# Optimization experiments

Hardware: AMD Instinct MI355X
Metric: run time of the kernel (lower is better)

Reference implementation:

```python
import jax, jax.numpy as jnp
import numpy as np

N = 8192        # n_nodes
F = 256         # n_features
RES_H = 512     # n_res_hidden
REP_H = 256     # n_rep_hidden
EMB = 128       # embed_dim
E = 262144      # n_edges
GAMMA = 0.1


def setup_inputs() -> dict:
    key = jax.random.key(0)
    ks = jax.random.split(key, 20)
    w = lambda k, shape, s=0.05: (jax.random.normal(k, shape, jnp.float32) * s)
    return {
        "x": jax.random.normal(ks[0], (N, F), jnp.float32),
        "edge_index": jax.random.randint(ks[1], (2, E), 0, N),
        # res_model: Linear(N,RES_H)+ReLU, Linear(RES_H,F)+ReLU
        "res_W1": w(ks[2], (N, RES_H)), "res_b1": jnp.zeros((RES_H,), jnp.float32),
        "res_W2": w(ks[3], (RES_H, F)), "res_b2": jnp.zeros((F,), jnp.float32),
        "fc_W1": w(ks[4], (F, REP_H)), "fc_b1": jnp.zeros((REP_H,), jnp.float32),
        "fc_W2": w(ks[5], (REP_H, REP_H)), "fc_b2": jnp.zeros((REP_H,), jnp.float32),
        # rep_gcn: GCNConv(F,REP_H,norm=False), GCNConv(REP_H,REP_H), GCNConv(REP_H,EMB)
        "g_W0": w(ks[6], (F, REP_H)), "g_b0": jnp.zeros((REP_H,), jnp.float32),
        "g_W1": w(ks[7], (REP_H, REP_H)), "g_b1": jnp.zeros((REP_H,), jnp.float32),
        "g_W2": w(ks[8], (REP_H, EMB)), "g_b2": jnp.zeros((EMB,), jnp.float32),
        # dec_fc: Linear(EMB,REP_H)+ReLU, Linear(REP_H,F)+ReLU
        "dec_W1": w(ks[9], (EMB, REP_H)), "dec_b1": jnp.zeros((REP_H,), jnp.float32),
        "dec_W2": w(ks[10], (REP_H, F)), "dec_b2": jnp.zeros((F,), jnp.float32),
    }


def _gcn(h, src, dst, W, b, normalize):
    """PyG GCNConv: transform then aggregate src->dst; sym-norm with self loops if normalize."""
    h = h @ W
    if normalize:
        ones = jnp.ones(src.shape[0], h.dtype)
        deg = jax.ops.segment_sum(ones, dst, num_segments=N) + 1.0  # +1 self loop
        dinv = jax.lax.rsqrt(deg)
        coef = dinv[src] * dinv[dst]
        agg = jax.ops.segment_sum(h[src] * coef[:, None], dst, num_segments=N)
        agg = agg + h * (dinv * dinv)[:, None]  # self-loop message
    else:
        agg = jax.ops.segment_sum(h[src], dst, num_segments=N)
    return agg + b


def _fwd(x, edge_index, res_W1, res_b1, res_W2, res_b2, fc_W1, fc_b1, fc_W2, fc_b2,
         g_W0, g_b0, g_W1, g_b1, g_W2, g_b2, dec_W1, dec_b1, dec_W2, dec_b2):
    relu = jax.nn.relu
    src, dst = edge_index[0], edge_index[1]
    # dense adjacency (to_dense_adj accumulates edge weights = 1)
    A = jnp.zeros((N, N), x.dtype).at[src, dst].add(1.0)
    # residual model over adjacency rows
    R = relu(relu(A @ res_W1 + res_b1) @ res_W2 + res_b2)  # [N, F]
    # GCN layer 0 (normalize=False)
    H = relu(_gcn(x, src, dst, g_W0, g_b0, False))
    # layer 1
    R_l = relu(R @ fc_W1 + fc_b1)
    H = relu(_gcn(H * jnp.exp(-GAMMA * R_l), src, dst, g_W1, g_b1, True))
    # layer 2
    R_l = relu(R_l @ fc_W2 + fc_b2)
    H = relu(_gcn(H * jnp.exp(-GAMMA * R_l), src, dst, g_W2, g_b2, True))  # [N, EMB]
    X_hat = relu(relu(H @ dec_W1 + dec_b1) @ dec_W2 + dec_b2)  # [N, F]
    A_hat = H @ H.T  # [N, N]
    return X_hat, A_hat, R


def reference(x, edge_index, res_W1, res_b1, res_W2, res_b2, fc_W1, fc_b1, fc_W2, fc_b2,
              g_W0, g_b0, g_W1, g_b1, g_W2, g_b2, dec_W1, dec_b1, dec_W2, dec_b2):
    return _fwd(x, edge_index, res_W1, res_b1, res_W2, res_b2, fc_W1, fc_b1, fc_W2, fc_b2,
                g_W0, g_b0, g_W1, g_b1, g_W2, g_b2, dec_W1, dec_b1, dec_W2, dec_b2)
```

## Files before the change

### kernel.cpp

```cpp
#include <hip/hip_runtime.h>
#include <cstddef>
#include <cstdint>
#include <math.h>

#define NN   8192
#define FF   256
#define RESH 512
#define REPH 256
#define EMBD 128
#define EE   262144
#define GAMMA_ 0.1f

typedef __attribute__((ext_vector_type(8))) short bf16x8;
typedef __attribute__((ext_vector_type(4))) float f32x4;
typedef __attribute__((ext_vector_type(2))) float f32x2;
typedef __attribute__((ext_vector_type(4))) short s16x4;
typedef __attribute__((ext_vector_type(2))) short s16x2;

__device__ inline void f2hilo(float x, short& h, short& l) {
  unsigned u = __float_as_uint(x);
  unsigned r = u + 0x7FFFu + ((u >> 16) & 1u);
  h = (short)(r >> 16);
  float hf = __uint_as_float(r & 0xFFFF0000u);
  float lf = x - hf;
  unsigned u2 = __float_as_uint(lf);
  unsigned r2 = u2 + 0x7FFFu + ((u2 >> 16) & 1u);
  l = (short)(r2 >> 16);
}


__global__ void count_kernel(const int* __restrict__ ei, int* __restrict__ cnt_src,
                             int* __restrict__ cnt_dst) {
  int e = blockIdx.x * blockDim.x + threadIdx.x;
  if (e < EE) {
    atomicAdd(&cnt_src[ei[e]], 1);
    atomicAdd(&cnt_dst[ei[EE + e]], 1);
  }
}

__global__ void scan_kernel(const int* __restrict__ cnt_src, const int* __restrict__ cnt_dst,
                            int* __restrict__ off_src, int* __restrict__ off_dst,
                            float* __restrict__ dinv) {
  const int* cnt = blockIdx.x ? cnt_dst : cnt_src;
  int* off = blockIdx.x ? off_dst : off_src;
  __shared__ int sm[1024];
  int carry = 0;
  for (int ch = 0; ch < NN / 1024; ++ch) {
    int idx = ch * 1024 + threadIdx.x;
    int v = cnt[idx];
    if (blockIdx.x) dinv[idx] = rsqrtf((float)v + 1.0f);
    int x = v;
    sm[threadIdx.x] = x;
    __syncthreads();
    for (int ofs = 1; ofs < 1024; ofs <<= 1) {
      int y = (threadIdx.x >= ofs) ? sm[threadIdx.x - ofs] : 0;
      __syncthreads();
      x += y;
      sm[threadIdx.x] = x;
      __syncthreads();
    }
    off[idx] = x - v + carry;
    carry += sm[1023];
    __syncthreads();
  }
  if (threadIdx.x == 0) off[NN] = carry;
}

__global__ void fill_kernel(const int* __restrict__ ei, const int* __restrict__ off_src,
                            const int* __restrict__ off_dst, int* __restrict__ cur_src,
                            int* __restrict__ cur_dst, int* __restrict__ adj_src,
                            int* __restrict__ adj_dst) {
  int e = blockIdx.x * blockDim.x + threadIdx.x;
  if (e < EE) {
    int s = ei[e], d = ei[EE + e];
    int ps = atomicAdd(&cur_src[s], 1);
    adj_src[off_src[s] + ps] = d;
    int pd = atomicAdd(&cur_dst[d], 1);
    adj_dst[off_dst[d] + pd] = s;
  }
}

__global__ __launch_bounds__(256) void s1_v2(const float* __restrict__ W1,
    const float* __restrict__ b1, const int* __restrict__ off_src,
    const int* __restrict__ adj_src, short* __restrict__ S1h, short* __restrict__ S1l) {
  __shared__ f32x4 p2[2][64];
  const int i = blockIdx.x, w = threadIdx.x >> 6, lane = threadIdx.x & 63;
  const int half = w & 1, par = w >> 1;
  const int col = half * 256 + lane * 4;
  const float* base = W1 + col;
  const int beg = off_src[i], end = off_src[i + 1];
  f32x4 acc = {};
  int k = beg + par;
  for (; k + 6 < end; k += 8) {
    int s0 = adj_src[k], s1 = adj_src[k + 2], s2 = adj_src[k + 4], s3 = adj_src[k + 6];
    f32x4 h0 = *(const f32x4*)(base + (size_t)s0 * RESH);
    f32x4 h1 = *(const f32x4*)(base + (size_t)s1 * RESH);
    f32x4 h2 = *(const f32x4*)(base + (size_t)s2 * RESH);
    f32x4 h3 = *(const f32x4*)(base + (size_t)s3 * RESH);
    acc += h0 + h1 + h2 + h3;
  }
  for (; k < end; k += 2) {
    int s = adj_src[k];
    acc += *(const f32x4*)(base + (size_t)s * RESH);
  }
  if (par == 1) p2[half][lane] = acc;
  __syncthreads();
  if (par == 0) {
    acc += p2[half][lane];
    f32x4 bb = *(const f32x4*)(b1 + col);
    s16x4 vh, vl;
#pragma unroll
    for (int j = 0; j < 4; ++j) {
      float v = fmaxf(acc[j] + bb[j], 0.f);
      short hh, ll;
      f2hilo(v, hh, ll);
      vh[j] = hh; vl[j] = ll;
    }
    size_t o = (size_t)i * RESH + col;
    *(s16x4*)(S1h + o) = vh;
    *(s16x4*)(S1l + o) = vl;
  }
}

__global__ __launch_bounds__(256) void agg0_v2(const float* __restrict__ h,
    const float* __restrict__ b, const float* __restrict__ mod,
    const int* __restrict__ off_dst, const int* __restrict__ adj_dst,
    short* __restrict__ oh, short* __restrict__ ol) {
  __shared__ f32x4 part[3][64];
  const int d = blockIdx.x, w = threadIdx.x >> 6, lane = threadIdx.x & 63;
  const float* base = h + lane * 4;
  const int beg = off_dst[d], end = off_dst[d + 1];
  f32x4 acc = {};
  int k = beg + w;
  for (; k + 12 < end; k += 16) {
    int s0 = adj_dst[k], s1 = adj_dst[k + 4], s2 = adj_dst[k + 8], s3 = adj_dst[k + 12];
    f32x4 h0 = *(const f32x4*)(base + (size_t)s0 * REPH);
    f32x4 h1 = *(const f32x4*)(base + (size_t)s1 * REPH);
    f32x4 h2 = *(const f32x4*)(base + (size_t)s2 * REPH);
    f32x4 h3 = *(const f32x4*)(base + (size_t)s3 * REPH);
    acc += h0 + h1 + h2 + h3;
  }
  for (; k < end; k += 4) {
    int s = adj_dst[k];
    acc += *(const f32x4*)(base + (size_t)s * REPH);
  }
  if (w) part[w - 1][lane] = acc;
  __syncthreads();
  if (w == 0) {
    acc += part[0][lane] + part[1][lane] + part[2][lane];
    size_t o = (size_t)d * REPH + lane * 4;
    f32x4 bb = *(const f32x4*)(b + lane * 4);
    f32x4 mm = *(const f32x4*)(mod + o);
    s16x4 vh, vl;
#pragma unroll
    for (int j = 0; j < 4; ++j) {
      float v = fmaxf(acc[j] + bb[j], 0.f) * expf(-GAMMA_ * mm[j]);
      short hh, ll;
      f2hilo(v, hh, ll);
      vh[j] = hh; vl[j] = ll;
    }
    *(s16x4*)(oh + o) = vh;
    *(s16x4*)(ol + o) = vl;
  }
}

__global__ __launch_bounds__(256) void aggn256_v2(const float* __restrict__ h,
    const float* __restrict__ b, const float* __restrict__ dinv,
    const float* __restrict__ mod, const int* __restrict__ off_dst,
    const int* __restrict__ adj_dst, short* __restrict__ oh, short* __restrict__ ol) {
  __shared__ f32x4 part[3][64];
  const int d = blockIdx.x, w = threadIdx.x >> 6, lane = threadIdx.x & 63;
  const float* base = h + lane * 4;
  const int beg = off_dst[d], end = off_dst[d + 1];
  f32x4 acc = {};
  int k = beg + w;
  for (; k + 12 < end; k += 16) {
    int s0 = adj_dst[k], s1 = adj_dst[k + 4], s2 = adj_dst[k + 8], s3 = adj_dst[k + 12];
    float d0 = dinv[s0], d1 = dinv[s1], d2 = dinv[s2], d3 = dinv[s3];
    f32x4 h0 = *(const f32x4*)(base + (size_t)s0 * REPH);
    f32x4 h1 = *(const f32x4*)(base + (size_t)s1 * REPH);
    f32x4 h2 = *(const f32x4*)(base + (size_t)s2 * REPH);
    f32x4 h3 = *(const f32x4*)(base + (size_t)s3 * REPH);
    acc += h0 * d0 + h1 * d1 + h2 * d2 + h3 * d3;
  }
  for (; k < end; k += 4) {
    int s = adj_dst[k];
    acc += *(const f32x4*)(base + (size_t)s * REPH) * dinv[s];
  }
  if (w) part[w - 1][lane] = acc;
  __syncthreads();
  if (w == 0) {
    acc += part[0][lane] + part[1][lane] + part[2][lane];
    const float dd = dinv[d];
    size_t o = (size_t)d * REPH + lane * 4;
    f32x4 bb = *(const f32x4*)(b + lane * 4);
    f32x4 self = *(const f32x4*)(h + o);
    s16x4 vh, vl;
    if (mod) {
      f32x4 mm = *(const f32x4*)(mod + o);
#pragma unroll
      for (int j = 0; j < 4; ++j) {
        float v = fmaxf(acc[j] * dd + self[j] * dd * dd + bb[j], 0.f) * expf(-GAMMA_ * mm[j]);
        short hh, ll; f2hilo(v, hh, ll); vh[j] = hh; vl[j] = ll;
      }
    } else {
#pragma unroll
      for (int j = 0; j < 4; ++j) {
        float v = fmaxf(acc[j] * dd + self[j] * dd * dd + bb[j], 0.f);
        short hh, ll; f2hilo(v, hh, ll); vh[j] = hh; vl[j] = ll;
      }
    }
    *(s16x4*)(oh + o) = vh;
    *(s16x4*)(ol + o) = vl;
  }
}

__global__ __launch_bounds__(256) void aggn128_v2(const float* __restrict__ h,
    const float* __restrict__ b, const float* __restrict__ dinv,
    const int* __restrict__ off_dst, const int* __restrict__ adj_dst,
    short* __restrict__ oh, short* __restrict__ ol) {
  __shared__ f32x2 part[3][64];
  const int d = blockIdx.x, w = threadIdx.x >> 6, lane = threadIdx.x & 63;
  const float* base = h + lane * 2;
  const int beg = off_dst[d], end = off_dst[d + 1];
  f32x2 acc = {};
  int k = beg + w;
  for (; k + 12 < end; k += 16) {
    int s0 = adj_dst[k], s1 = adj_dst[k + 4], s2 = adj_dst[k + 8], s3 = adj_dst[k + 12];
    float d0 = dinv[s0], d1 = dinv[s1], d2 = dinv[s2], d3 = dinv[s3];
    f32x2 h0 = *(const f32x2*)(base + (size_t)s0 * EMBD);
    f32x2 h1 = *(const f32x2*)(base + (size_t)s1 * EMBD);
    f32x2 h2 = *(const f32x2*)(base + (size_t)s2 * EMBD);
    f32x2 h3 = *(const f32x2*)(base + (size_t)s3 * EMBD);
    acc += h0 * d0 + h1 * d1 + h2 * d2 + h3 * d3;
  }
  for (; k < end; k += 4) {
    int s = adj_dst[k];
    acc += *(const f32x2*)(base + (size_t)s * EMBD) * dinv[s];
  }
  if (w) part[w - 1][lane] = acc;
  __syncthreads();
  if (w == 0) {
    acc += part[0][lane] + part[1][lane] + part[2][lane];
    const float dd = dinv[d];
    size_t o = (size_t)d * EMBD + lane * 2;
    f32x2 bb = *(const f32x2*)(b + lane * 2);
    f32x2 self = *(const f32x2*)(h + o);
    s16x2 vh, vl;
#pragma unroll
    for (int j = 0; j < 2; ++j) {
      float v = fmaxf(acc[j] * dd + self[j] * dd * dd + bb[j], 0.f);
      short hh, ll; f2hilo(v, hh, ll); vh[j] = hh; vl[j] = ll;
    }
    *(s16x2*)(oh + o) = vh;
    *(s16x2*)(ol + o) = vl;
  }
}

struct WDesc { const float* src; short* h; short* l; int K; int N; };
struct WTab { WDesc d[8]; };

__global__ void prep_w(WTab tab) {
  WDesc d = tab.d[blockIdx.y];
  int total = d.K * d.N;
  for (int i = blockIdx.x * 256 + threadIdx.x; i < total; i += 128 * 256) {
    int n = i / d.K, k = i - n * d.K;
    float x = d.src[(size_t)k * d.N + n];
    short hh, ll;
    f2hilo(x, hh, ll);
    d.h[i] = hh;
    d.l[i] = ll;
  }
}

__global__ void conv_split(const float* __restrict__ in, short* __restrict__ oh,
                           short* __restrict__ ol) {
  int i = (blockIdx.x * 256 + threadIdx.x) * 4;
  f32x4 v = *(const f32x4*)(in + i);
  s16x4 vh, vl;
#pragma unroll
  for (int j = 0; j < 4; ++j) {
    short hh, ll;
    f2hilo(v[j], hh, ll);
    vh[j] = hh;
    vl[j] = ll;
  }
  *(s16x4*)(oh + i) = vh;
  *(s16x4*)(ol + i) = vl;
}

template<int CB>
__global__ __launch_bounds__(256) void gemmS(const short* __restrict__ Ah,
    const short* __restrict__ Al, const short* __restrict__ Wh,
    const short* __restrict__ Wl, const float* __restrict__ bias, int doRelu,
    float* __restrict__ outF, short* __restrict__ outH, short* __restrict__ outL,
    int K, int Nc) {
  const int w = threadIdx.x >> 6, l = threadIdx.x & 63;
  const int lr = l & 15, lk = l >> 4;
  const int m0 = blockIdx.y * 64 + w * 16;
  const int n0 = blockIdx.x * (CB * 16);
  f32x4 acc[CB] = {};
  const int nks = K >> 5;
  for (int ks = 0; ks < nks; ++ks) {
    const int k0 = (ks << 5) + (lk << 3);
    size_t aoff = (size_t)(m0 + lr) * K + k0;
    bf16x8 ah = *(const bf16x8*)(Ah + aoff);
    bf16x8 al = *(const bf16x8*)(Al + aoff);
#pragma unroll
    for (int cb = 0; cb < CB; ++cb) {
      size_t boff = (size_t)(n0 + (cb << 4) + lr) * K + k0;
      bf16x8 bh = *(const bf16x8*)(Wh + boff);
      bf16x8 bl = *(const bf16x8*)(Wl + boff);
      acc[cb] = __builtin_amdgcn_mfma_f32_16x16x32_bf16(ah, bh, acc[cb], 0, 0, 0);
      acc[cb] = __builtin_amdgcn_mfma_f32_16x16x32_bf16(al, bh, acc[cb], 0, 0, 0);
      acc[cb] = __builtin_amdgcn_mfma_f32_16x16x32_bf16(ah, bl, acc[cb], 0, 0, 0);
    }
  }
#pragma unroll
  for (int cb = 0; cb < CB; ++cb) {
    int col = n0 + (cb << 4) + lr;
    float bv = bias ? bias[col] : 0.f;
#pragma unroll
    for (int r = 0; r < 4; ++r) {
      int row = m0 + (lk << 2) + r;
      float v = acc[cb][r] + bv;
      if (doRelu) v = fmaxf(v, 0.f);
      size_t off = (size_t)row * Nc + col;
      if (outF) outF[off] = v;
      if (outH) {
        short hh, ll;
        f2hilo(v, hh, ll);
        outH[off] = hh;
        outL[off] = ll;
      }
    }
  }
}

__global__ __launch_bounds__(256) void ahat_sym(const short* __restrict__ Hh,
    const short* __restrict__ Hl, float* __restrict__ C) {
  __shared__ float sm[128][129];
  int z = blockIdx.x;
  int b = (int)((sqrtf(8.f * (float)z + 1.f) - 1.f) * 0.5f);
  while ((b + 1) * (b + 2) / 2 <= z) ++b;
  while (b * (b + 1) / 2 > z) --b;
  int a = z - b * (b + 1) / 2;
  const int bi = a * 128, bj = b * 128;
  const bool mirror = (a != b);
  const int w = threadIdx.x >> 6, l = threadIdx.x & 63;
  const int lr = l & 15, lk = l >> 4;
  const int ri = w * 32;
  f32x4 acc[2][8] = {};
#pragma unroll
  for (int ks = 0; ks < 4; ++ks) {
    const int k0 = (ks << 5) + (lk << 3);
    bf16x8 ah[2], al[2];
#pragma unroll
    for (int rb = 0; rb < 2; ++rb) {
      size_t off = (size_t)(bi + ri + (rb << 4) + lr) * EMBD + k0;
      ah[rb] = *(const bf16x8*)(Hh + off);
      al[rb] = *(const bf16x8*)(Hl + off);
    }
#pragma unroll
    for (int cb = 0; cb < 8; ++cb) {
      size_t off = (size_t)(bj + (cb << 4) + lr) * EMBD + k0;
      bf16x8 bh = *(const bf16x8*)(Hh + off);
      bf16x8 bl = *(const bf16x8*)(Hl + off);
#pragma unroll
      for (int rb = 0; rb < 2; ++rb) {
        acc[rb][cb] = __builtin_amdgcn_mfma_f32_16x16x32_bf16(ah[rb], bh, acc[rb][cb], 0, 0, 0);
        acc[rb][cb] = __builtin_amdgcn_mfma_f32_16x16x32_bf16(al[rb], bh, acc[rb][cb], 0, 0, 0);
        acc[rb][cb] = __builtin_amdgcn_mfma_f32_16x16x32_bf16(ah[rb], bl, acc[rb][cb], 0, 0, 0);
      }
    }
  }
#pragma unroll
  for (int rb = 0; rb < 2; ++rb)
#pragma unroll
    for (int cb = 0; cb < 8; ++cb) {
      int r0 = ri + (rb << 4) + (lk << 2);
      int c0 = (cb << 4) + lr;
#pragma unroll
      for (int r = 0; r < 4; ++r) {
        float v = acc[rb][cb][r];
        C[(size_t)(bi + r0 + r) * NN + bj + c0] = v;
        if (mirror) sm[r0 + r][c0] = v;
      }
    }
  if (mirror) {
    __syncthreads();
    for (int idx = threadIdx.x; idx < 128 * 128; idx += 256) {
      int jr = idx >> 7, c = idx & 127;
      C[(size_t)(bj + jr) * NN + bi + c] = sm[c][jr];
    }
  }
}


extern "C" void kernel_launch(void* const* d_in, const int* in_sizes, int n_in,
                              void* d_out, int out_size, void* d_ws, size_t ws_size,
                              hipStream_t stream) {
  const float* x      = (const float*)d_in[0];
  const int*   ei     = (const int*)d_in[1];
  const float* res_W1 = (const float*)d_in[2];
  const float* res_b1 = (const float*)d_in[3];
  const float* res_W2 = (const float*)d_in[4];
  const float* res_b2 = (const float*)d_in[5];
  const float* fc_W1  = (const float*)d_in[6];
  const float* fc_b1  = (const float*)d_in[7];
  const float* fc_W2  = (const float*)d_in[8];
  const float* fc_b2  = (const float*)d_in[9];
  const float* g_W0   = (const float*)d_in[10];
  const float* g_b0   = (const float*)d_in[11];
  const float* g_W1   = (const float*)d_in[12];
  const float* g_b1   = (const float*)d_in[13];
  const float* g_W2   = (const float*)d_in[14];
  const float* g_b2   = (const float*)d_in[15];
  const float* dec_W1 = (const float*)d_in[16];
  const float* dec_b1 = (const float*)d_in[17];
  const float* dec_W2 = (const float*)d_in[18];
  const float* dec_b2 = (const float*)d_in[19];

  float* out   = (float*)d_out;
  float* X_hat = out;
  float* A_hat = out + (size_t)NN * FF;
  float* R     = A_hat + (size_t)NN * NN;

  char* ws = (char*)d_ws;
  size_t o = 0;
  auto alloc = [&](size_t bytes) -> void* {
    void* p = ws + o;
    o += (bytes + 1023) & ~(size_t)1023;
    return p;
  };
  int* cnt_src = (int*)alloc(NN * 4);
  int* cnt_dst = (int*)alloc(NN * 4);
  int* cur_src = (int*)alloc(NN * 4);
  int* cur_dst = (int*)alloc(NN * 4);
  int* off_src = (int*)alloc((NN + 1) * 4);
  int* off_dst = (int*)alloc((NN + 1) * 4);
  int* adj_src = (int*)alloc((size_t)EE * 4);
  int* adj_dst = (int*)alloc((size_t)EE * 4);
  float* dinv  = (float*)alloc(NN * 4);
  short* Wt_h  = (short*)alloc(524288 * 2);
  short* Wt_l  = (short*)alloc(524288 * 2);
  const size_t SLAB = (size_t)8 * 1024 * 1024;
  char* slabA = (char*)alloc(SLAB);
  char* slabB = (char*)alloc(SLAB);
  char* slabC = (char*)alloc(SLAB);
  char* slabD = (char*)alloc(SLAB);
  short* S1h = (short*)slabA;
  short* Xh  = (short*)slabA;            short* Xl  = (short*)(slabA + SLAB / 2);
  short* M1h = (short*)slabA;            short* M1l = (short*)(slabA + SLAB / 2);
  short* M2h = (short*)slabA;            short* M2l = (short*)(slabA + SLAB / 2);
  short* D1h = (short*)slabA;            short* D1l = (short*)(slabA + SLAB / 2);
  short* S1l = (short*)slabB;
  float* B3f = (float*)slabB;
  float* B4f = (float*)slabB;
  float* G2f = (float*)slabB;
  short* Rh  = (short*)slabC;            short* Rl  = (short*)(slabC + SLAB / 2);
  float* B1f = (float*)slabC;
  float* G1f = (float*)slabC;
  short* B3h = (short*)slabD;            short* B3l = (short*)(slabD + SLAB / 2);
  short* Hh  = (short*)slabD;            short* Hl  = (short*)(slabD + (size_t)2 * 1024 * 1024);

  const int o_resW2 = 0;
  const int o_fcW1  = 131072;
  const int o_fcW2  = 196608;
  const int o_gW0   = 262144;
  const int o_gW1   = 327680;
  const int o_gW2   = 393216;
  const int o_decW1 = 425984;
  const int o_decW2 = 458752;

  hipMemsetAsync(cnt_src, 0, (size_t)NN * 4 * 4, stream);

  count_kernel<<<EE / 256, 256, 0, stream>>>(ei, cnt_src, cnt_dst);
  scan_kernel<<<2, 1024, 0, stream>>>(cnt_src, cnt_dst, off_src, off_dst, dinv);
  fill_kernel<<<EE / 256, 256, 0, stream>>>(ei, off_src, off_dst, cur_src, cur_dst,
                                            adj_src, adj_dst);

  WTab tab;
  tab.d[0] = {res_W2, Wt_h + o_resW2, Wt_l + o_resW2, RESH, FF};
  tab.d[1] = {fc_W1,  Wt_h + o_fcW1,  Wt_l + o_fcW1,  FF,   REPH};
  tab.d[2] = {fc_W2,  Wt_h + o_fcW2,  Wt_l + o_fcW2,  REPH, REPH};
  tab.d[3] = {g_W0,   Wt_h + o_gW0,   Wt_l + o_gW0,   FF,   REPH};
  tab.d[4] = {g_W1,   Wt_h + o_gW1,   Wt_l + o_gW1,   REPH, REPH};
  tab.d[5] = {g_W2,   Wt_h + o_gW2,   Wt_l + o_gW2,   REPH, EMBD};
  tab.d[6] = {dec_W1, Wt_h + o_decW1, Wt_l + o_decW1, EMBD, REPH};
  tab.d[7] = {dec_W2, Wt_h + o_decW2, Wt_l + o_decW2, REPH, FF};
  prep_w<<<dim3(128, 8), 256, 0, stream>>>(tab);

  s1_v2<<<NN, 256, 0, stream>>>(res_W1, res_b1, off_src, adj_src, S1h, S1l);
  gemmS<8><<<dim3(2, 128), 256, 0, stream>>>(S1h, S1l, Wt_h + o_resW2, Wt_l + o_resW2,
      res_b2, 1, R, Rh, Rl, RESH, FF);
  gemmS<8><<<dim3(2, 128), 256, 0, stream>>>(Rh, Rl, Wt_h + o_fcW1, Wt_l + o_fcW1,
      fc_b1, 1, B3f, B3h, B3l, FF, REPH);
  conv_split<<<(NN * FF) / 1024, 256, 0, stream>>>(x, Xh, Xl);
  gemmS<8><<<dim3(2, 128), 256, 0, stream>>>(Xh, Xl, Wt_h + o_gW0, Wt_l + o_gW0,
      nullptr, 0, B1f, nullptr, nullptr, FF, REPH);
  agg0_v2<<<NN, 256, 0, stream>>>(B1f, g_b0, B3f, off_dst, adj_dst, M1h, M1l);
  gemmS<8><<<dim3(2, 128), 256, 0, stream>>>(M1h, M1l, Wt_h + o_gW1, Wt_l + o_gW1,
      nullptr, 0, G1f, nullptr, nullptr, REPH, REPH);
  gemmS<8><<<dim3(2, 128), 256, 0, stream>>>(B3h, B3l, Wt_h + o_fcW2, Wt_l + o_fcW2,
      fc_b2, 1, B4f, nullptr, nullptr, REPH, REPH);
  aggn256_v2<<<NN, 256, 0, stream>>>(G1f, g_b1, dinv, B4f, off_dst, adj_dst, M2h, M2l);
  gemmS<4><<<dim3(2, 128), 256, 0, stream>>>(M2h, M2l, Wt_h + o_gW2, Wt_l + o_gW2,
      nullptr, 0, G2f, nullptr, nullptr, REPH, EMBD);
  aggn128_v2<<<NN, 256, 0, stream>>>(G2f, g_b2, dinv, off_dst, adj_dst, Hh, Hl);
  gemmS<8><<<dim3(2, 128), 256, 0, stream>>>(Hh, Hl, Wt_h + o_decW1, Wt_l + o_decW1,
      dec_b1, 1, nullptr, D1h, D1l, EMBD, REPH);
  gemmS<8><<<dim3(2, 128), 256, 0, stream>>>(D1h, D1l, Wt_h + o_decW2, Wt_l + o_decW2,
      dec_b2, 1, X_hat, nullptr, nullptr, REPH, FF);
  ahat_sym<<<2080, 256, 0, stream>>>(Hh, Hl, A_hat);
}
```

Before: 787.5 us.

## Partition gathers into source-range phases, widen GEMM grids, vectorize A_hat stores

The sparse gathers (s1, agg0, aggn256) now run as several passes, each accepting only source nodes inside a 2048- or 4096-node window. The goal is to keep the gathered rows resident in cache, and partial sums go through an fp32 scratch buffer between passes. GEMM launches use a smaller column block with twice as many blocks, and the conversion of x to bf16 is folded into the weight-prep kernel. The A_hat writer stages the tile in LDS and writes float4 rows for both the tile and its mirror. In exchange, the adjacency lists are rescanned once per pass and each pass reads and writes partial sums.

```diff
diff --git a/kernel.cpp b/kernel.cpp
--- a/kernel.cpp
+++ b/kernel.cpp
@@ -80,9 +80,10 @@
   }
 }
 
-__global__ __launch_bounds__(256) void s1_v2(const float* __restrict__ W1,
+__global__ __launch_bounds__(256) void s1_ph(const float* __restrict__ W1,
     const float* __restrict__ b1, const int* __restrict__ off_src,
-    const int* __restrict__ adj_src, short* __restrict__ S1h, short* __restrict__ S1l) {
+    const int* __restrict__ adj_src, float* __restrict__ S1f,
+    short* __restrict__ S1h, short* __restrict__ S1l, int lo, int first, int last) {
   __shared__ f32x4 p2[2][64];
   const int i = blockIdx.x, w = threadIdx.x >> 6, lane = threadIdx.x & 63;
   const int half = w & 1, par = w >> 1;
@@ -93,39 +94,44 @@
   int k = beg + par;
   for (; k + 6 < end; k += 8) {
     int s0 = adj_src[k], s1 = adj_src[k + 2], s2 = adj_src[k + 4], s3 = adj_src[k + 6];
-    f32x4 h0 = *(const f32x4*)(base + (size_t)s0 * RESH);
-    f32x4 h1 = *(const f32x4*)(base + (size_t)s1 * RESH);
-    f32x4 h2 = *(const f32x4*)(base + (size_t)s2 * RESH);
-    f32x4 h3 = *(const f32x4*)(base + (size_t)s3 * RESH);
-    acc += h0 + h1 + h2 + h3;
+    if ((unsigned)(s0 - lo) < 2048u) acc += *(const f32x4*)(base + (size_t)s0 * RESH);
+    if ((unsigned)(s1 - lo) < 2048u) acc += *(const f32x4*)(base + (size_t)s1 * RESH);
+    if ((unsigned)(s2 - lo) < 2048u) acc += *(const f32x4*)(base + (size_t)s2 * RESH);
+    if ((unsigned)(s3 - lo) < 2048u) acc += *(const f32x4*)(base + (size_t)s3 * RESH);
   }
   for (; k < end; k += 2) {
     int s = adj_src[k];
-    acc += *(const f32x4*)(base + (size_t)s * RESH);
+    if ((unsigned)(s - lo) < 2048u) acc += *(const f32x4*)(base + (size_t)s * RESH);
   }
   if (par == 1) p2[half][lane] = acc;
   __syncthreads();
   if (par == 0) {
     acc += p2[half][lane];
-    f32x4 bb = *(const f32x4*)(b1 + col);
-    s16x4 vh, vl;
-#pragma unroll
-    for (int j = 0; j < 4; ++j) {
-      float v = fmaxf(acc[j] + bb[j], 0.f);
-      short hh, ll;
-      f2hilo(v, hh, ll);
-      vh[j] = hh; vl[j] = ll;
-    }
     size_t o = (size_t)i * RESH + col;
-    *(s16x4*)(S1h + o) = vh;
-    *(s16x4*)(S1l + o) = vl;
-  }
-}
-
-__global__ __launch_bounds__(256) void agg0_v2(const float* __restrict__ h,
+    if (!first) acc += *(const f32x4*)(S1f + o);
+    if (!last) {
+      *(f32x4*)(S1f + o) = acc;
+    } else {
+      f32x4 bb = *(const f32x4*)(b1 + col);
+      s16x4 vh, vl;
+#pragma unroll
+      for (int j = 0; j < 4; ++j) {
+        float v = fmaxf(acc[j] + bb[j], 0.f);
+        short hh, ll;
+        f2hilo(v, hh, ll);
+        vh[j] = hh; vl[j] = ll;
+      }
+      *(s16x4*)(S1h + o) = vh;
+      *(s16x4*)(S1l + o) = vl;
+    }
+  }
+}
+
+__global__ __launch_bounds__(256) void agg0_ph(const float* __restrict__ h,
     const float* __restrict__ b, const float* __restrict__ mod,
     const int* __restrict__ off_dst, const int* __restrict__ adj_dst,
-    short* __restrict__ oh, short* __restrict__ ol) {
+    float* __restrict__ Pf, short* __restrict__ oh, short* __restrict__ ol,
+    int lo, int first, int last) {
   __shared__ f32x4 part[3][64];
   const int d = blockIdx.x, w = threadIdx.x >> 6, lane = threadIdx.x & 63;
   const float* base = h + lane * 4;
@@ -134,40 +140,45 @@
   int k = beg + w;
   for (; k + 12 < end; k += 16) {
     int s0 = adj_dst[k], s1 = adj_dst[k + 4], s2 = adj_dst[k + 8], s3 = adj_dst[k + 12];
-    f32x4 h0 = *(const f32x4*)(base + (size_t)s0 * REPH);
-    f32x4 h1 = *(const f32x4*)(base + (size_t)s1 * REPH);
-    f32x4 h2 = *(const f32x4*)(base + (size_t)s2 * REPH);
-    f32x4 h3 = *(const f32x4*)(base + (size_t)s3 * REPH);
-    acc += h0 + h1 + h2 + h3;
+    if ((unsigned)(s0 - lo) < 4096u) acc += *(const f32x4*)(base + (size_t)s0 * REPH);
+    if ((unsigned)(s1 - lo) < 4096u) acc += *(const f32x4*)(base + (size_t)s1 * REPH);
+    if ((unsigned)(s2 - lo) < 4096u) acc += *(const f32x4*)(base + (size_t)s2 * REPH);
+    if ((unsigned)(s3 - lo) < 4096u) acc += *(const f32x4*)(base + (size_t)s3 * REPH);
   }
   for (; k < end; k += 4) {
     int s = adj_dst[k];
-    acc += *(const f32x4*)(base + (size_t)s * REPH);
+    if ((unsigned)(s - lo) < 4096u) acc += *(const f32x4*)(base + (size_t)s * REPH);
   }
   if (w) part[w - 1][lane] = acc;
   __syncthreads();
   if (w == 0) {
     acc += part[0][lane] + part[1][lane] + part[2][lane];
     size_t o = (size_t)d * REPH + lane * 4;
-    f32x4 bb = *(const f32x4*)(b + lane * 4);
-    f32x4 mm = *(const f32x4*)(mod + o);
-    s16x4 vh, vl;
-#pragma unroll
-    for (int j = 0; j < 4; ++j) {
-      float v = fmaxf(acc[j] + bb[j], 0.f) * expf(-GAMMA_ * mm[j]);
-      short hh, ll;
-      f2hilo(v, hh, ll);
-      vh[j] = hh; vl[j] = ll;
-    }
-    *(s16x4*)(oh + o) = vh;
-    *(s16x4*)(ol + o) = vl;
-  }
-}
-
-__global__ __launch_bounds__(256) void aggn256_v2(const float* __restrict__ h,
+    if (!first) acc += *(const f32x4*)(Pf + o);
+    if (!last) {
+      *(f32x4*)(Pf + o) = acc;
+    } else {
+      f32x4 bb = *(const f32x4*)(b + lane * 4);
+      f32x4 mm = *(const f32x4*)(mod + o);
+      s16x4 vh, vl;
+#pragma unroll
+      for (int j = 0; j < 4; ++j) {
+        float v = fmaxf(acc[j] + bb[j], 0.f) * expf(-GAMMA_ * mm[j]);
+        short hh, ll;
+        f2hilo(v, hh, ll);
+        vh[j] = hh; vl[j] = ll;
+      }
+      *(s16x4*)(oh + o) = vh;
+      *(s16x4*)(ol + o) = vl;
+    }
+  }
+}
+
+__global__ __launch_bounds__(256) void aggn256_ph(const float* __restrict__ h,
     const float* __restrict__ b, const float* __restrict__ dinv,
     const float* __restrict__ mod, const int* __restrict__ off_dst,
-    const int* __restrict__ adj_dst, short* __restrict__ oh, short* __restrict__ ol) {
+    const int* __restrict__ adj_dst, float* __restrict__ Pf,
+    short* __restrict__ oh, short* __restrict__ ol, int lo, int first, int last) {
   __shared__ f32x4 part[3][64];
   const int d = blockIdx.x, w = threadIdx.x >> 6, lane = threadIdx.x & 63;
   const float* base = h + lane * 4;
@@ -176,42 +187,39 @@
   int k = beg + w;
   for (; k + 12 < end; k += 16) {
     int s0 = adj_dst[k], s1 = adj_dst[k + 4], s2 = adj_dst[k + 8], s3 = adj_dst[k + 12];
-    float d0 = dinv[s0], d1 = dinv[s1], d2 = dinv[s2], d3 = dinv[s3];
-    f32x4 h0 = *(const f32x4*)(base + (size_t)s0 * REPH);
-    f32x4 h1 = *(const f32x4*)(base + (size_t)s1 * REPH);
-    f32x4 h2 = *(const f32x4*)(base + (size_t)s2 * REPH);
-    f32x4 h3 = *(const f32x4*)(base + (size_t)s3 * REPH);
-    acc += h0 * d0 + h1 * d1 + h2 * d2 + h3 * d3;
+    if ((unsigned)(s0 - lo) < 4096u) acc += *(const f32x4*)(base + (size_t)s0 * REPH) * dinv[s0];
+    if ((unsigned)(s1 - lo) < 4096u) acc += *(const f32x4*)(base + (size_t)s1 * REPH) * dinv[s1];
+    if ((unsigned)(s2 - lo) < 4096u) acc += *(const f32x4*)(base + (size_t)s2 * REPH) * dinv[s2];
+    if ((unsigned)(s3 - lo) < 4096u) acc += *(const f32x4*)(base + (size_t)s3 * REPH) * dinv[s3];
   }
   for (; k < end; k += 4) {
     int s = adj_dst[k];
-    acc += *(const f32x4*)(base + (size_t)s * REPH) * dinv[s];
+    if ((unsigned)(s - lo) < 4096u) acc += *(const f32x4*)(base + (size_t)s * REPH) * dinv[s];
   }
   if (w) part[w - 1][lane] = acc;
   __syncthreads();
   if (w == 0) {
     acc += part[0][lane] + part[1][lane] + part[2][lane];
-    const float dd = dinv[d];
     size_t o = (size_t)d * REPH + lane * 4;
-    f32x4 bb = *(const f32x4*)(b + lane * 4);
-    f32x4 self = *(const f32x4*)(h + o);
-    s16x4 vh, vl;
-    if (mod) {
+    if (!first) acc += *(const f32x4*)(Pf + o);
+    if (!last) {
+      *(f32x4*)(Pf + o) = acc;
+    } else {
+      const float dd = dinv[d];
+      f32x4 bb = *(const f32x4*)(b + lane * 4);
+      f32x4 self = *(const f32x4*)(h + o);
       f32x4 mm = *(const f32x4*)(mod + o);
+      s16x4 vh, vl;
 #pragma unroll
       for (int j = 0; j < 4; ++j) {
         float v = fmaxf(acc[j] * dd + self[j] * dd * dd + bb[j], 0.f) * expf(-GAMMA_ * mm[j]);
-        short hh, ll; f2hilo(v, hh, ll); vh[j] = hh; vl[j] = ll;
+        short hh, ll;
+        f2hilo(v, hh, ll);
+        vh[j] = hh; vl[j] = ll;
       }
-    } else {
-#pragma unroll
-      for (int j = 0; j < 4; ++j) {
-        float v = fmaxf(acc[j] * dd + self[j] * dd * dd + bb[j], 0.f);
-        short hh, ll; f2hilo(v, hh, ll); vh[j] = hh; vl[j] = ll;
-      }
-    }
-    *(s16x4*)(oh + o) = vh;
-    *(s16x4*)(ol + o) = vl;
+      *(s16x4*)(oh + o) = vh;
+      *(s16x4*)(ol + o) = vl;
+    }
   }
 }
 
@@ -257,36 +265,25 @@
   }
 }
 
-struct WDesc { const float* src; short* h; short* l; int K; int N; };
-struct WTab { WDesc d[8]; };
+struct WDesc { const float* src; short* h; short* l; int K; int N; int tr; };
+struct WTab { WDesc d[9]; };
 
 __global__ void prep_w(WTab tab) {
   WDesc d = tab.d[blockIdx.y];
   int total = d.K * d.N;
   for (int i = blockIdx.x * 256 + threadIdx.x; i < total; i += 128 * 256) {
-    int n = i / d.K, k = i - n * d.K;
-    float x = d.src[(size_t)k * d.N + n];
+    float x;
+    if (d.tr) {
+      int n = i / d.K, k = i - n * d.K;
+      x = d.src[(size_t)k * d.N + n];
+    } else {
+      x = d.src[i];
+    }
     short hh, ll;
     f2hilo(x, hh, ll);
     d.h[i] = hh;
     d.l[i] = ll;
   }
-}
-
-__global__ void conv_split(const float* __restrict__ in, short* __restrict__ oh,
-                           short* __restrict__ ol) {
-  int i = (blockIdx.x * 256 + threadIdx.x) * 4;
-  f32x4 v = *(const f32x4*)(in + i);
-  s16x4 vh, vl;
-#pragma unroll
-  for (int j = 0; j < 4; ++j) {
-    short hh, ll;
-    f2hilo(v[j], hh, ll);
-    vh[j] = hh;
-    vl[j] = ll;
-  }
-  *(s16x4*)(oh + i) = vh;
-  *(s16x4*)(ol + i) = vl;
 }
 
 template<int CB>
@@ -339,7 +336,7 @@
 
 __global__ __launch_bounds__(256) void ahat_sym(const short* __restrict__ Hh,
     const short* __restrict__ Hl, float* __restrict__ C) {
-  __shared__ float sm[128][129];
+  __shared__ float sm[128][132];
   int z = blockIdx.x;
   int b = (int)((sqrtf(8.f * (float)z + 1.f) - 1.f) * 0.5f);
   while ((b + 1) * (b + 2) / 2 <= z) ++b;
@@ -381,17 +378,21 @@
       int r0 = ri + (rb << 4) + (lk << 2);
       int c0 = (cb << 4) + lr;
 #pragma unroll
-      for (int r = 0; r < 4; ++r) {
-        float v = acc[rb][cb][r];
-        C[(size_t)(bi + r0 + r) * NN + bj + c0] = v;
-        if (mirror) sm[r0 + r][c0] = v;
-      }
-    }
+      for (int r = 0; r < 4; ++r) sm[r0 + r][c0] = acc[rb][cb][r];
+    }
+  __syncthreads();
+  for (int idx = threadIdx.x; idx < 128 * 32; idx += 256) {
+    int row = idx >> 5, c4 = (idx & 31) << 2;
+    float4 v = *(const float4*)&sm[row][c4];
+    *(float4*)&C[(size_t)(bi + row) * NN + bj + c4] = v;
+  }
   if (mirror) {
-    __syncthreads();
-    for (int idx = threadIdx.x; idx < 128 * 128; idx += 256) {
-      int jr = idx >> 7, c = idx & 127;
-      C[(size_t)(bj + jr) * NN + bi + c] = sm[c][jr];
+    for (int idx = threadIdx.x; idx < 128 * 32; idx += 256) {
+      int row = idx >> 5, c4 = (idx & 31) << 2;
+      float4 v;
+      v.x = sm[c4 + 0][row]; v.y = sm[c4 + 1][row];
+      v.z = sm[c4 + 2][row]; v.w = sm[c4 + 3][row];
+      *(float4*)&C[(size_t)(bj + row) * NN + bi + c4] = v;
     }
   }
 }
@@ -433,6 +434,7 @@
     o += (bytes + 1023) & ~(size_t)1023;
     return p;
   };
+  const size_t MB = 1024 * 1024;
   int* cnt_src = (int*)alloc(NN * 4);
   int* cnt_dst = (int*)alloc(NN * 4);
   int* cur_src = (int*)alloc(NN * 4);
@@ -444,25 +446,33 @@
   float* dinv  = (float*)alloc(NN * 4);
   short* Wt_h  = (short*)alloc(524288 * 2);
   short* Wt_l  = (short*)alloc(524288 * 2);
-  const size_t SLAB = (size_t)8 * 1024 * 1024;
-  char* slabA = (char*)alloc(SLAB);
-  char* slabB = (char*)alloc(SLAB);
-  char* slabC = (char*)alloc(SLAB);
-  char* slabD = (char*)alloc(SLAB);
-  short* S1h = (short*)slabA;
-  short* Xh  = (short*)slabA;            short* Xl  = (short*)(slabA + SLAB / 2);
-  short* M1h = (short*)slabA;            short* M1l = (short*)(slabA + SLAB / 2);
-  short* M2h = (short*)slabA;            short* M2l = (short*)(slabA + SLAB / 2);
-  short* D1h = (short*)slabA;            short* D1l = (short*)(slabA + SLAB / 2);
-  short* S1l = (short*)slabB;
-  float* B3f = (float*)slabB;
-  float* B4f = (float*)slabB;
-  float* G2f = (float*)slabB;
-  short* Rh  = (short*)slabC;            short* Rl  = (short*)(slabC + SLAB / 2);
-  float* B1f = (float*)slabC;
-  float* G1f = (float*)slabC;
-  short* B3h = (short*)slabD;            short* B3l = (short*)(slabD + SLAB / 2);
-  short* Hh  = (short*)slabD;            short* Hl  = (short*)(slabD + (size_t)2 * 1024 * 1024);
+  char* bS1f = (char*)alloc(16 * MB);
+  char* bS1h = (char*)alloc(8 * MB);
+  char* bS1l = (char*)alloc(8 * MB);
+  char* bX   = (char*)alloc(8 * MB);
+  char* bR   = (char*)alloc(8 * MB);
+  char* bB3f = (char*)alloc(8 * MB);
+  char* bB3  = (char*)alloc(8 * MB);
+  char* bB1f = (char*)alloc(8 * MB);
+  char* bPf  = (char*)alloc(8 * MB);
+  char* bM1  = (char*)alloc(8 * MB);
+  char* bG2f = (char*)alloc(4 * MB);
+  char* bH   = (char*)alloc(4 * MB);
+
+  float* S1f = (float*)bS1f;           float* G1f = (float*)bS1f;
+  short* S1h = (short*)bS1h;           short* D1h = (short*)bS1h;
+  short* S1l = (short*)bS1l;           short* D1l = (short*)bS1l;
+  short* Xh  = (short*)bX;             short* Xl  = (short*)(bX + 4 * MB);
+  float* B4f = (float*)bX;
+  short* Rh  = (short*)bR;             short* Rl  = (short*)(bR + 4 * MB);
+  short* M2h = (short*)bR;             short* M2l = (short*)(bR + 4 * MB);
+  float* B3f = (float*)bB3f;
+  short* B3h = (short*)bB3;            short* B3l = (short*)(bB3 + 4 * MB);
+  float* B1f = (float*)bB1f;
+  float* Pf  = (float*)bPf;
+  short* M1h = (short*)bM1;            short* M1l = (short*)(bM1 + 4 * MB);
+  float* G2f = (float*)bG2f;
+  short* Hh  = (short*)bH;             short* Hl  = (short*)(bH + 2 * MB);
 
   const int o_resW2 = 0;
   const int o_fcW1  = 131072;
@@ -481,36 +491,43 @@
                                             adj_src, adj_dst);
 
   WTab tab;
-  tab.d[0] = {res_W2, Wt_h + o_resW2, Wt_l + o_resW2, RESH, FF};
-  tab.d[1] = {fc_W1,  Wt_h + o_fcW1,  Wt_l + o_fcW1,  FF,   REPH};
-  tab.d[2] = {fc_W2,  Wt_h + o_fcW2,  Wt_l + o_fcW2,  REPH, REPH};
-  tab.d[3] = {g_W0,   Wt_h + o_gW0,   Wt_l + o_gW0,   FF,   REPH};
-  tab.d[4] = {g_W1,   Wt_h + o_gW1,   Wt_l + o_gW1,   REPH, REPH};
-  tab.d[5] = {g_W2,   Wt_h + o_gW2,   Wt_l + o_gW2,   REPH, EMBD};
-  tab.d[6] = {dec_W1, Wt_h + o_decW1, Wt_l + o_decW1, EMBD, REPH};
-  tab.d[7] = {dec_W2, Wt_h + o_decW2, Wt_l + o_decW2, REPH, FF};
-  prep_w<<<dim3(128, 8), 256, 0, stream>>>(tab);
-
-  s1_v2<<<NN, 256, 0, stream>>>(res_W1, res_b1, off_src, adj_src, S1h, S1l);
-  gemmS<8><<<dim3(2, 128), 256, 0, stream>>>(S1h, S1l, Wt_h + o_resW2, Wt_l + o_resW2,
+  tab.d[0] = {res_W2, Wt_h + o_resW2, Wt_l + o_resW2, RESH, FF,   1};
+  tab.d[1] = {fc_W1,  Wt_h + o_fcW1,  Wt_l + o_fcW1,  FF,   REPH, 1};
+  tab.d[2] = {fc_W2,  Wt_h + o_fcW2,  Wt_l + o_fcW2,  REPH, REPH, 1};
+  tab.d[3] = {g_W0,   Wt_h + o_gW0,   Wt_l + o_gW0,   FF,   REPH, 1};
+  tab.d[4] = {g_W1,   Wt_h + o_gW1,   Wt_l + o_gW1,   REPH, REPH, 1};
+  tab.d[5] = {g_W2,   Wt_h + o_gW2,   Wt_l + o_gW2,   REPH, EMBD, 1};
+  tab.d[6] = {dec_W1, Wt_h + o_decW1, Wt_l + o_decW1, EMBD, REPH, 1};
+  tab.d[7] = {dec_W2, Wt_h + o_decW2, Wt_l + o_decW2, REPH, FF,   1};
+  tab.d[8] = {x,      Xh,             Xl,             FF,   NN,   0};
+  prep_w<<<dim3(128, 9), 256, 0, stream>>>(tab);
+
+  s1_ph<<<NN, 256, 0, stream>>>(res_W1, res_b1, off_src, adj_src, S1f, S1h, S1l, 0,    1, 0);
+  s1_ph<<<NN, 256, 0, stream>>>(res_W1, res_b1, off_src, adj_src, S1f, S1h, S1l, 2048, 0, 0);
+  s1_ph<<<NN, 256, 0, stream>>>(res_W1, res_b1, off_src, adj_src, S1f, S1h, S1l, 4096, 0, 0);
+  s1_ph<<<NN, 256, 0, stream>>>(res_W1, res_b1, off_src, adj_src, S1f, S1h, S1l, 6144, 0, 1);
+  gemmS<4><<<dim3(4, 128), 256, 0, stream>>>(S1h, S1l, Wt_h + o_resW2, Wt_l + o_resW2,
       res_b2, 1, R, Rh, Rl, RESH, FF);
-  gemmS<8><<<dim3(2, 128), 256, 0, stream>>>(Rh, Rl, Wt_h + o_fcW1, Wt_l + o_fcW1,
+  gemmS<4><<<dim3(4, 128), 256, 0, stream>>>(Rh, Rl, Wt_h + o_fcW1, Wt_l + o_fcW1,
       fc_b1, 1, B3f, B3h, B3l, FF, REPH);
-  conv_split<<<(NN * FF) / 1024, 256, 0, stream>>>(x, Xh, Xl);
-  gemmS<8><<<dim3(2, 128), 256, 0, stream>>>(Xh, Xl, Wt_h + o_gW0, Wt_l + o_gW0,
+  gemmS<4><<<dim3(4, 128), 256, 0, stream>>>(Xh, Xl, Wt_h + o_gW0, Wt_l + o_gW0,
       nullptr, 0, B1f, nullptr, nullptr, FF, REPH);
-  agg0_v2<<<NN, 256, 0, stream>>>(B1f, g_b0, B3f, off_dst, adj_dst, M1h, M1l);
-  gemmS<8><<<dim3(2, 128), 256, 0, stream>>>(M1h, M1l, Wt_h + o_gW1, Wt_l + o_gW1,
+  agg0_ph<<<NN, 256, 0, stream>>>(B1f, g_b0, B3f, off_dst, adj_dst, Pf, M1h, M1l, 0,    1, 0);
+  agg0_ph<<<NN, 256, 0, stream>>>(B1f, g_b0, B3f, off_dst, adj_dst, Pf, M1h, M1l, 4096, 0, 1);
+  gemmS<4><<<dim3(4, 128), 256, 0, stream>>>(M1h, M1l, Wt_h + o_gW1, Wt_l + o_gW1,
       nullptr, 0, G1f, nullptr, nullptr, REPH, REPH);
-  gemmS<8><<<dim3(2, 128), 256, 0, stream>>>(B3h, B3l, Wt_h + o_fcW2, Wt_l + o_fcW2,
+  gemmS<4><<<dim3(4, 128), 256, 0, stream>>>(B3h, B3l, Wt_h + o_fcW2, Wt_l + o_fcW2,
       fc_b2, 1, B4f, nullptr, nullptr, REPH, REPH);
-  aggn256_v2<<<NN, 256, 0, stream>>>(G1f, g_b1, dinv, B4f, off_dst, adj_dst, M2h, M2l);
-  gemmS<4><<<dim3(2, 128), 256, 0, stream>>>(M2h, M2l, Wt_h + o_gW2, Wt_l + o_gW2,
+  aggn256_ph<<<NN, 256, 0, stream>>>(G1f, g_b1, dinv, B4f, off_dst, adj_dst, Pf,
+                                     M2h, M2l, 0,    1, 0);
+  aggn256_ph<<<NN, 256, 0, stream>>>(G1f, g_b1, dinv, B4f, off_dst, adj_dst, Pf,
+                                     M2h, M2l, 4096, 0, 1);
+  gemmS<2><<<dim3(4, 128), 256, 0, stream>>>(M2h, M2l, Wt_h + o_gW2, Wt_l + o_gW2,
       nullptr, 0, G2f, nullptr, nullptr, REPH, EMBD);
   aggn128_v2<<<NN, 256, 0, stream>>>(G2f, g_b2, dinv, off_dst, adj_dst, Hh, Hl);
-  gemmS<8><<<dim3(2, 128), 256, 0, stream>>>(Hh, Hl, Wt_h + o_decW1, Wt_l + o_decW1,
+  gemmS<4><<<dim3(4, 128), 256, 0, stream>>>(Hh, Hl, Wt_h + o_decW1, Wt_l + o_decW1,
       dec_b1, 1, nullptr, D1h, D1l, EMBD, REPH);
-  gemmS<8><<<dim3(2, 128), 256, 0, stream>>>(D1h, D1l, Wt_h + o_decW2, Wt_l + o_decW2,
+  gemmS<4><<<dim3(4, 128), 256, 0, stream>>>(D1h, D1l, Wt_h + o_decW2, Wt_l + o_decW2,
       dec_b2, 1, X_hat, nullptr, nullptr, REPH, FF);
   ahat_sym<<<2080, 256, 0, stream>>>(Hh, Hl, A_hat);
 }
```

Result: slower. 869.2 us (+10.4%).
